# Optimization experiments

Hardware: AMD Instinct MI355X
Metric: run time of the kernel (lower is better)

## Reference

```python
import jax, jax.numpy as jnp
import numpy as np

B = 65536
HIDDEN = 200
K = 10          # num codewords == codeword dim (NearestEmbed(k, emb_size=k))
GROUPS = HIDDEN // K  # 20 sub-vectors of dim K per sample


def setup_inputs() -> dict:
    key = jax.random.key(0)
    ks = jax.random.split(key, 10)
    s = 0.05  # small init scale
    return {
        "x": jax.random.uniform(ks[0], (B, 784), dtype=jnp.float32),
        "W1": jax.random.normal(ks[1], (400, 784), dtype=jnp.float32) * s,
        "b1": jnp.zeros((400,), dtype=jnp.float32),
        "W2": jax.random.normal(ks[2], (HIDDEN, 400), dtype=jnp.float32) * s,
        "b2": jnp.zeros((HIDDEN,), dtype=jnp.float32),
        "W3": jax.random.normal(ks[3], (400, HIDDEN), dtype=jnp.float32) * s,
        "b3": jnp.zeros((400,), dtype=jnp.float32),
        "W4": jax.random.normal(ks[4], (784, 400), dtype=jnp.float32) * s,
        "b4": jnp.zeros((784,), dtype=jnp.float32),
        "codebook": jax.random.normal(ks[5], (K, K), dtype=jnp.float32),  # (n_codes, code_dim)
    }


def _quantize(z, codebook):
    # z: (B, K, GROUPS) -- quantize each length-K column vector to nearest codeword.
    v = jnp.transpose(z, (0, 2, 1))                       # (B, G, K)
    d2 = (jnp.sum(v * v, -1, keepdims=True)
          - 2.0 * jnp.einsum('bgk,ck->bgc', v, codebook)
          + jnp.sum(codebook * codebook, -1))             # (B, G, C)
    idx = jnp.argmin(d2, axis=-1)                         # (B, G)
    q = codebook[idx]                                     # (B, G, K) gather
    return jnp.transpose(q, (0, 2, 1)), idx               # (B, K, G)


def reference(x, W1, b1, W2, b2, W3, b3, W4, b4, codebook):
    # encode
    h1 = jax.nn.relu(x @ W1.T + b1)                       # (B, 400)
    z_e_flat = h1 @ W2.T + b2                             # (B, 200)
    z_e = z_e_flat.reshape(B, K, GROUPS)                  # (B, 10, 20)

    # z_q: straight-through quantization, codebook grad stopped (weight_sg=True)
    q, _ = _quantize(z_e, codebook)
    z_q = (z_e + jax.lax.stop_gradient(q - z_e)).reshape(B, HIDDEN)

    # emb: quantize detached z_e; gradient flows only to codebook via gather
    q2, _ = _quantize(jax.lax.stop_gradient(z_e), codebook)
    emb = q2.reshape(B, HIDDEN)

    # decode (original uses tanh on the output)
    h3 = jax.nn.relu(z_q @ W3.T + b3)                     # (B, 400)
    recon = jnp.tanh(h3 @ W4.T + b4)                      # (B, 784)
    return recon, z_e, emb
```

## Files before the change

kernel.cpp:

```cpp
#include <hip/hip_runtime.h>
#include <hip/hip_bf16.h>

#define NB   65536
#define KD   10
#define NG   20
#define NH   200
#define NH1  400
#define NIN  784

#define TAU 3e-4

using short8 = __attribute__((ext_vector_type(8))) short;
using f32x4  = __attribute__((ext_vector_type(4))) float;

__device__ inline float bf2f(unsigned short u) {
  union { unsigned int i; float f; } x; x.i = ((unsigned int)u) << 16; return x.f;
}
__device__ inline unsigned short f2bf(float v) {
  __hip_bfloat16 b = __float2bfloat16(v);
  return *reinterpret_cast<unsigned short*>(&b);
}
__device__ inline void gload_lds16(const void* g, void* l) {
  __builtin_amdgcn_global_load_lds(
      (const __attribute__((address_space(1))) unsigned int*)g,
      (__attribute__((address_space(3))) unsigned int*)l, 16, 0, 0);
}

__global__ __launch_bounds__(256) void gemm1_fused(
    const float* __restrict__ xf,
    const unsigned short* __restrict__ Bhi, const unsigned short* __restrict__ Blo,
    const float* __restrict__ bias,
    unsigned short* __restrict__ Ohi, unsigned short* __restrict__ Olo)
{
  __shared__ __align__(16) short As_hi[2][128][32];
  __shared__ __align__(16) short As_lo[2][128][32];
  __shared__ __align__(16) short Bs_hi[2][128][32];
  __shared__ __align__(16) short Bs_lo[2][128][32];
  const int tid = threadIdx.x;
  const int lane = tid & 63, wid = tid >> 6;
  const int wr = wid >> 1, wc = wid & 1;
  const int bid = blockIdx.x;
  const int sw = (bid & 7) * 256 + (bid >> 3);
  const int n0 = (sw & 3) * 128;
  const int m0 = (sw >> 2) * 128;
  const int rr = lane >> 2, kofs = (lane & 3) * 8;
  const int arow = tid >> 3;
  const int acol = (tid & 7) * 4;

  f32x4 acc[4][4];
  #pragma unroll
  for (int i = 0; i < 4; ++i)
    #pragma unroll
    for (int j = 0; j < 4; ++j) acc[i][j] = (f32x4){0.f, 0.f, 0.f, 0.f};

  float4 va[4];

  auto loadA = [&](int ks) {
    const int k0 = ks * 32;
    #pragma unroll
    for (int p = 0; p < 4; ++p) {
      const int row = p * 32 + arow;
      const int kk = k0 + acol;
      va[p] = make_float4(0.f, 0.f, 0.f, 0.f);
      if (kk < NIN)
        va[p] = *reinterpret_cast<const float4*>(xf + (size_t)(m0 + row) * NIN + kk);
    }
  };
  auto stageB = [&](int ks, int buf) {
    const int k0 = ks * 32;
    #pragma unroll
    for (int c = 0; c < 4; ++c) {
      const int ch = wid * 4 + c;
      if (ch < 8)
        gload_lds16(Bhi + (size_t)(n0 + ch * 16 + rr) * 800 + k0 + kofs,
                    (char*)&Bs_hi[buf][0][0] + ch * 1024);
      else
        gload_lds16(Blo + (size_t)(n0 + (ch - 8) * 16 + rr) * 800 + k0 + kofs,
                    (char*)&Bs_lo[buf][0][0] + (ch - 8) * 1024);
    }
  };
  auto writeA = [&](int buf) {
    #pragma unroll
    for (int p = 0; p < 4; ++p) {
      const int row = p * 32 + arow;
      const float4 v = va[p];
      short4 h, l;
      h.x = (short)f2bf(v.x); l.x = (short)f2bf(v.x - bf2f((unsigned short)h.x));
      h.y = (short)f2bf(v.y); l.y = (short)f2bf(v.y - bf2f((unsigned short)h.y));
      h.z = (short)f2bf(v.z); l.z = (short)f2bf(v.z - bf2f((unsigned short)h.z));
      h.w = (short)f2bf(v.w); l.w = (short)f2bf(v.w - bf2f((unsigned short)h.w));
      *reinterpret_cast<short4*>(&As_hi[buf][row][acol]) = h;
      *reinterpret_cast<short4*>(&As_lo[buf][row][acol]) = l;
    }
  };

  loadA(0);
  stageB(0, 0);
  writeA(0);
  __syncthreads();

  for (int ks = 0; ks < 25; ++ks) {
    const int cur = ks & 1, nxt = cur ^ 1;
    const bool more = (ks + 1 < 25);
    if (more) {
      loadA(ks + 1);
      stageB(ks + 1, nxt);
    }
    short8 ah[4], al[4], bh[4], bl[4];
    #pragma unroll
    for (int i = 0; i < 4; ++i) {
      ah[i] = *reinterpret_cast<const short8*>(&As_hi[cur][wr * 64 + i * 16 + (lane & 15)][(lane >> 4) * 8]);
      al[i] = *reinterpret_cast<const short8*>(&As_lo[cur][wr * 64 + i * 16 + (lane & 15)][(lane >> 4) * 8]);
      bh[i] = *reinterpret_cast<const short8*>(&Bs_hi[cur][wc * 64 + i * 16 + (lane & 15)][(lane >> 4) * 8]);
      bl[i] = *reinterpret_cast<const short8*>(&Bs_lo[cur][wc * 64 + i * 16 + (lane & 15)][(lane >> 4) * 8]);
    }
    #pragma unroll
    for (int i = 0; i < 4; ++i)
      #pragma unroll
      for (int j = 0; j < 4; ++j) {
        acc[i][j] = __builtin_amdgcn_mfma_f32_16x16x32_bf16(ah[i], bh[j], acc[i][j], 0, 0, 0);
        acc[i][j] = __builtin_amdgcn_mfma_f32_16x16x32_bf16(al[i], bh[j], acc[i][j], 0, 0, 0);
        acc[i][j] = __builtin_amdgcn_mfma_f32_16x16x32_bf16(ah[i], bl[j], acc[i][j], 0, 0, 0);
      }
    if (more) writeA(nxt);
    __syncthreads();
  }

  #pragma unroll
  for (int j = 0; j < 4; ++j) {
    const int n = n0 + wc * 64 + j * 16 + (lane & 15);
    if (n >= NH1) continue;
    const float bn = bias[n];
    #pragma unroll
    for (int i = 0; i < 4; ++i) {
      const int mb = m0 + wr * 64 + i * 16 + (lane >> 4) * 4;
      #pragma unroll
      for (int r = 0; r < 4; ++r) {
        float v = fmaxf(acc[i][j][r] + bn, 0.f);
        unsigned short h = f2bf(v);
        Ohi[(size_t)(mb + r) * NH1 + n] = h;
        Olo[(size_t)(mb + r) * NH1 + n] = f2bf(v - bf2f(h));
      }
    }
  }
}

__global__ __launch_bounds__(256) void gemm2_split(
    const unsigned short* __restrict__ Ahi, const unsigned short* __restrict__ Alo,
    const unsigned short* __restrict__ Bhi, const unsigned short* __restrict__ Blo,
    const unsigned short* __restrict__ zp, const float* __restrict__ bias,
    float* __restrict__ Of)
{
  __shared__ __align__(16) short As_hi[128][32];
  __shared__ __align__(16) short As_lo[128][32];
  __shared__ __align__(16) short Bs_hi[128][32];
  __shared__ __align__(16) short Bs_lo[128][32];
  const int tid = threadIdx.x;
  const int lane = tid & 63, wid = tid >> 6;
  const int wr = wid >> 1, wc = wid & 1;
  const int bid = blockIdx.x;
  const int sw = (bid & 7) * 128 + (bid >> 3);
  const int n0 = (sw & 1) * 128;
  const int m0 = (sw >> 1) * 128;

  const unsigned short* G = (wid == 0) ? Ahi : (wid == 1) ? Alo
                          : (wid == 2) ? Bhi : Blo;
  short* Lt = (wid == 0) ? &As_hi[0][0] : (wid == 1) ? &As_lo[0][0]
            : (wid == 2) ? &Bs_hi[0][0] : &Bs_lo[0][0];
  const bool isA = wid < 2;
  const int rbase = isA ? m0 : n0;
  const int ld = isA ? 400 : 416;
  const int rr = lane >> 2;
  const int kofs = (lane & 3) * 8;

  f32x4 acc[4][4];
  #pragma unroll
  for (int i = 0; i < 4; ++i)
    #pragma unroll
    for (int j = 0; j < 4; ++j) acc[i][j] = (f32x4){0.f, 0.f, 0.f, 0.f};

  for (int ks = 0; ks < 13; ++ks) {
    const int k0 = ks * 32;
    #pragma unroll
    for (int c = 0; c < 8; ++c) {
      const unsigned short* src =
          G + (size_t)(rbase + c * 16 + rr) * ld + k0 + kofs;
      if (isA && (k0 + kofs >= 400)) src = zp;
      gload_lds16(src, (char*)Lt + c * 1024);
    }
    __syncthreads();
    short8 ah[4], al[4], bh[4], bl[4];
    #pragma unroll
    for (int i = 0; i < 4; ++i) {
      ah[i] = *reinterpret_cast<const short8*>(&As_hi[wr * 64 + i * 16 + (lane & 15)][(lane >> 4) * 8]);
      al[i] = *reinterpret_cast<const short8*>(&As_lo[wr * 64 + i * 16 + (lane & 15)][(lane >> 4) * 8]);
      bh[i] = *reinterpret_cast<const short8*>(&Bs_hi[wc * 64 + i * 16 + (lane & 15)][(lane >> 4) * 8]);
      bl[i] = *reinterpret_cast<const short8*>(&Bs_lo[wc * 64 + i * 16 + (lane & 15)][(lane >> 4) * 8]);
    }
    #pragma unroll
    for (int i = 0; i < 4; ++i)
      #pragma unroll
      for (int j = 0; j < 4; ++j) {
        acc[i][j] = __builtin_amdgcn_mfma_f32_16x16x32_bf16(ah[i], bh[j], acc[i][j], 0, 0, 0);
        acc[i][j] = __builtin_amdgcn_mfma_f32_16x16x32_bf16(al[i], bh[j], acc[i][j], 0, 0, 0);
        acc[i][j] = __builtin_amdgcn_mfma_f32_16x16x32_bf16(ah[i], bl[j], acc[i][j], 0, 0, 0);
      }
    __syncthreads();
  }

  #pragma unroll
  for (int j = 0; j < 4; ++j) {
    const int n = n0 + wc * 64 + j * 16 + (lane & 15);
    if (n >= NH) continue;
    const float bn = bias[n];
    #pragma unroll
    for (int i = 0; i < 4; ++i) {
      const int mb = m0 + wr * 64 + i * 16 + (lane >> 4) * 4;
      #pragma unroll
      for (int r = 0; r < 4; ++r)
        Of[(size_t)(mb + r) * NH + n] = acc[i][j][r] + bn;
    }
  }
}

__global__ __launch_bounds__(256) void gemm3_mfma(
    const unsigned short* __restrict__ A,
    const __hip_bfloat16* __restrict__ Bp,
    const float* __restrict__ bias, __hip_bfloat16* __restrict__ H3)
{
  __shared__ __align__(16) short As[128][32];
  __shared__ __align__(16) short Bs[128][32];
  const int tid = threadIdx.x;
  const int lane = tid & 63, wid = tid >> 6;
  const int wr = wid >> 1, wc = wid & 1;
  const int bid = blockIdx.x;
  const int sw = (bid & 7) * 256 + (bid >> 3);
  const int n0 = (sw & 3) * 128;
  const int m0 = (sw >> 2) * 128;
  const int srow = lane >> 2;
  const int skp  = (lane & 3) * 8;
  const short* Ag = (const short*)A;
  const short* Bg = (const short*)Bp;
  f32x4 acc[4][4];
  #pragma unroll
  for (int i = 0; i < 4; ++i)
    #pragma unroll
    for (int j = 0; j < 4; ++j) acc[i][j] = (f32x4){0.f, 0.f, 0.f, 0.f};

  for (int k0 = 0; k0 < 224; k0 += 32) {
    #pragma unroll
    for (int c = 0; c < 2; ++c) {
      const int row = c * 64 + wid * 16 + srow;
      gload_lds16(Ag + (size_t)(m0 + row) * 200 + k0 + skp,
                  (char*)&As[0][0] + c * 4096 + wid * 1024);
      gload_lds16(Bg + (size_t)(n0 + row) * 224 + k0 + skp,
                  (char*)&Bs[0][0] + c * 4096 + wid * 1024);
    }
    __syncthreads();
    short8 af[4], bf[4];
    #pragma unroll
    for (int i = 0; i < 4; ++i)
      af[i] = *reinterpret_cast<const short8*>(&As[wr * 64 + i * 16 + (lane & 15)][(lane >> 4) * 8]);
    #pragma unroll
    for (int j = 0; j < 4; ++j)
      bf[j] = *reinterpret_cast<const short8*>(&Bs[wc * 64 + j * 16 + (lane & 15)][(lane >> 4) * 8]);
    #pragma unroll
    for (int i = 0; i < 4; ++i)
      #pragma unroll
      for (int j = 0; j < 4; ++j)
        acc[i][j] = __builtin_amdgcn_mfma_f32_16x16x32_bf16(af[i], bf[j], acc[i][j], 0, 0, 0);
    __syncthreads();
  }

  #pragma unroll
  for (int j = 0; j < 4; ++j) {
    const int n = n0 + wc * 64 + j * 16 + (lane & 15);
    if (n >= NH1) continue;
    const float bn = bias[n];
    #pragma unroll
    for (int i = 0; i < 4; ++i) {
      const int mb = m0 + wr * 64 + i * 16 + (lane >> 4) * 4;
      #pragma unroll
      for (int r = 0; r < 4; ++r)
        H3[(size_t)(mb + r) * NH1 + n] = __float2bfloat16(fmaxf(acc[i][j][r] + bn, 0.f));
    }
  }
}

__global__ __launch_bounds__(256) void gemm5_mfma(
    const __hip_bfloat16* __restrict__ A,
    const __hip_bfloat16* __restrict__ Bp,
    const float* __restrict__ bias, float* __restrict__ C)
{
  __shared__ __align__(16) short As[128][32];
  __shared__ __align__(16) short Bs[128][32];
  const int tid = threadIdx.x;
  const int lane = tid & 63, wid = tid >> 6;
  const int wr = wid >> 1, wc = wid & 1;
  const int bid = blockIdx.x;
  const int sw = (bid & 7) * 448 + (bid >> 3);
  const int n0 = (sw % 7) * 128;
  const int m0 = (sw / 7) * 128;
  const int srow = lane >> 2;
  const int skp  = (lane & 3) * 8;
  const short* Ag = (const short*)A;
  const short* Bg = (const short*)Bp;
  f32x4 acc[4][4];
  #pragma unroll
  for (int i = 0; i < 4; ++i)
    #pragma unroll
    for (int j = 0; j < 4; ++j) acc[i][j] = (f32x4){0.f, 0.f, 0.f, 0.f};

  for (int k0 = 0; k0 < 416; k0 += 32) {
    #pragma unroll
    for (int c = 0; c < 2; ++c) {
      const int row = c * 64 + wid * 16 + srow;
      gload_lds16(Ag + (size_t)(m0 + row) * 400 + k0 + skp,
                  (char*)&As[0][0] + c * 4096 + wid * 1024);
      gload_lds16(Bg + (size_t)(n0 + row) * 416 + k0 + skp,
                  (char*)&Bs[0][0] + c * 4096 + wid * 1024);
    }
    __syncthreads();
    short8 af[4], bf[4];
    #pragma unroll
    for (int i = 0; i < 4; ++i)
      af[i] = *reinterpret_cast<const short8*>(&As[wr * 64 + i * 16 + (lane & 15)][(lane >> 4) * 8]);
    #pragma unroll
    for (int j = 0; j < 4; ++j)
      bf[j] = *reinterpret_cast<const short8*>(&Bs[wc * 64 + j * 16 + (lane & 15)][(lane >> 4) * 8]);
    #pragma unroll
    for (int i = 0; i < 4; ++i)
      #pragma unroll
      for (int j = 0; j < 4; ++j)
        acc[i][j] = __builtin_amdgcn_mfma_f32_16x16x32_bf16(af[i], bf[j], acc[i][j], 0, 0, 0);
    __syncthreads();
  }

  #pragma unroll
  for (int j = 0; j < 4; ++j) {
    const int n = n0 + wc * 64 + j * 16 + (lane & 15);
    if (n >= NIN) continue;
    const float bn = bias[n];
    #pragma unroll
    for (int i = 0; i < 4; ++i) {
      const int mb = m0 + wr * 64 + i * 16 + (lane >> 4) * 4;
      #pragma unroll
      for (int r = 0; r < 4; ++r)
        C[(size_t)(mb + r) * NIN + n] = tanhf(acc[i][j][r] + bn);
    }
  }
}

__global__ __launch_bounds__(256) void conv_w(
    const float* __restrict__ W, unsigned short* __restrict__ Wh,
    unsigned short* __restrict__ Wl, int NP, int KP, int N, int K)
{
  const int i = blockIdx.x * 256 + threadIdx.x;
  if (i >= NP * KP) return;
  const int n = i / KP, k = i % KP;
  const float v = (n < N && k < K) ? W[(size_t)n * K + k] : 0.f;
  const unsigned short h = f2bf(v);
  Wh[i] = h;
  Wl[i] = f2bf(v - bf2f(h));
}

__global__ __launch_bounds__(256) void pad_w4(
    const float* __restrict__ W4, __hip_bfloat16* __restrict__ W4p)
{
  const int i = blockIdx.x * 256 + threadIdx.x;
  if (i >= 896 * 416) return;
  const int n = i / 416, k = i % 416;
  const float v = (n < NIN && k < NH1) ? W4[(size_t)n * NH1 + k] : 0.f;
  W4p[i] = __float2bfloat16(v);
}

__global__ __launch_bounds__(256) void pad_w3(
    const float* __restrict__ W3, __hip_bfloat16* __restrict__ W3p)
{
  const int i = blockIdx.x * 256 + threadIdx.x;
  if (i >= 512 * 224) return;
  const int n = i / 224, k = i % 224;
  const float v = (n < NH1 && k < NH) ? W3[(size_t)n * NH + k] : 0.f;
  W3p[i] = __float2bfloat16(v);
}

__global__ __launch_bounds__(256) void quant_kernel(
    const float* __restrict__ z_e, const float* __restrict__ cb,
    float* __restrict__ emb, unsigned short* __restrict__ ebf,
    unsigned char* __restrict__ sflag)
{
  __shared__ double cs[KD][KD];
  __shared__ double chalf[KD];
  __shared__ unsigned short cbf[KD][KD];
  const int tid = threadIdx.x;
  if (tid < KD * KD) {
    const double c = (double)cb[tid];
    cs[tid / KD][tid % KD] = c;
    cbf[tid / KD][tid % KD] = f2bf((float)c);
  }
  __syncthreads();
  if (tid < KD) {
    double s = 0.0;
    #pragma unroll
    for (int k = 0; k < KD; ++k) s += cs[tid][k] * cs[tid][k];
    chalf[tid] = 0.5 * s;
  }
  __syncthreads();

  const int gi = blockIdx.x * 256 + tid;
  const int b = gi / NG;
  const int g = gi % NG;
  const float* zrow = z_e + (size_t)b * NH + g;
  double v[KD];
  #pragma unroll
  for (int k = 0; k < KD; ++k) v[k] = (double)zrow[k * NG];

  int best = 0; double bt = 1e300, bt2 = 1e300;
  #pragma unroll
  for (int j = 0; j < KD; ++j) {
    double t = chalf[j];
    #pragma unroll
    for (int k = 0; k < KD; ++k) t -= v[k] * cs[j][k];
    if (t < bt) { bt2 = bt; bt = t; best = j; }
    else if (t < bt2) { bt2 = t; }
  }
  float* ep = emb + (size_t)b * NH + g;
  unsigned short* eb = ebf + (size_t)b * NH + g;
  #pragma unroll
  for (int k = 0; k < KD; ++k) {
    ep[k * NG] = (float)cs[best][k];
    eb[k * NG] = cbf[best][k];
  }
  if (bt2 - bt < TAU) sflag[b] = 1;
}

__global__ __launch_bounds__(256) void compact_kernel(
    const unsigned char* __restrict__ sflag, int* __restrict__ scount,
    int* __restrict__ slist)
{
  const int i = blockIdx.x * 256 + threadIdx.x;
  if (i < NB && sflag[i]) slist[atomicAdd(scount, 1)] = i;
}

__global__ __launch_bounds__(256) void repair_kernel(
    const float* __restrict__ x, const float* __restrict__ W1,
    const float* __restrict__ b1, const float* __restrict__ W2,
    const float* __restrict__ b2, const float* __restrict__ cb,
    const int* __restrict__ slist, const int* __restrict__ scount,
    float* __restrict__ emb, unsigned short* __restrict__ ebf)
{
  __shared__ double h1s[NH1];
  __shared__ double zs[NH];
  __shared__ double cs[KD][KD];
  __shared__ double chalf[KD];
  const int tid = threadIdx.x;
  const int lane = tid & 63, wv = tid >> 6;
  if (tid < KD * KD) cs[tid / KD][tid % KD] = (double)cb[tid];
  __syncthreads();
  if (tid < KD) {
    double s = 0.0;
    #pragma unroll
    for (int k = 0; k < KD; ++k) s += cs[tid][k] * cs[tid][k];
    chalf[tid] = 0.5 * s;
  }

  int S = *scount; if (S > NB) S = NB;

  for (int si = blockIdx.x; si < S; si += gridDim.x) {
    const int b = slist[si];
    double xr[4][4];
    #pragma unroll
    for (int it = 0; it < 4; ++it) {
      const int c4 = it * 64 + lane;
      if (c4 < 196) {
        float4 v = reinterpret_cast<const float4*>(x + (size_t)b * NIN)[c4];
        xr[it][0] = v.x; xr[it][1] = v.y; xr[it][2] = v.z; xr[it][3] = v.w;
      } else {
        xr[it][0] = xr[it][1] = xr[it][2] = xr[it][3] = 0.0;
      }
    }
    for (int j = wv; j < NH1; j += 4) {
      const float4* wr = reinterpret_cast<const float4*>(W1 + (size_t)j * NIN);
      double s0 = 0, s1 = 0, s2 = 0, s3 = 0;
      #pragma unroll
      for (int it = 0; it < 4; ++it) {
        const int c4 = it * 64 + lane;
        if (c4 < 196) {
          float4 w = wr[c4];
          s0 = fma(xr[it][0], (double)w.x, s0);
          s1 = fma(xr[it][1], (double)w.y, s1);
          s2 = fma(xr[it][2], (double)w.z, s2);
          s3 = fma(xr[it][3], (double)w.w, s3);
        }
      }
      double s = (s0 + s1) + (s2 + s3);
      #pragma unroll
      for (int off = 32; off > 0; off >>= 1) s += __shfl_down(s, off);
      if (lane == 0) { double h = s + (double)b1[j]; h1s[j] = h > 0.0 ? h : 0.0; }
    }
    __syncthreads();
    double hr[2][4];
    #pragma unroll
    for (int it = 0; it < 2; ++it) {
      const int c4 = it * 64 + lane;
      if (c4 < 100) {
        hr[it][0] = h1s[4 * c4 + 0]; hr[it][1] = h1s[4 * c4 + 1];
        hr[it][2] = h1s[4 * c4 + 2]; hr[it][3] = h1s[4 * c4 + 3];
      } else {
        hr[it][0] = hr[it][1] = hr[it][2] = hr[it][3] = 0.0;
      }
    }
    for (int n = wv; n < NH; n += 4) {
      const float4* wr = reinterpret_cast<const float4*>(W2 + (size_t)n * NH1);
      double s0 = 0, s1 = 0, s2 = 0, s3 = 0;
      #pragma unroll
      for (int it = 0; it < 2; ++it) {
        const int c4 = it * 64 + lane;
        if (c4 < 100) {
          float4 w = wr[c4];
          s0 = fma(hr[it][0], (double)w.x, s0);
          s1 = fma(hr[it][1], (double)w.y, s1);
          s2 = fma(hr[it][2], (double)w.z, s2);
          s3 = fma(hr[it][3], (double)w.w, s3);
        }
      }
      double s = (s0 + s1) + (s2 + s3);
      #pragma unroll
      for (int off = 32; off > 0; off >>= 1) s += __shfl_down(s, off);
      if (lane == 0) zs[n] = s + (double)b2[n];
    }
    __syncthreads();
    if (tid < NG) {
      const int g = tid;
      int best = 0; double bt = 1e300;
      #pragma unroll
      for (int j = 0; j < KD; ++j) {
        double t = chalf[j];
        #pragma unroll
        for (int k = 0; k < KD; ++k) t -= zs[k * NG + g] * cs[j][k];
        if (t < bt) { bt = t; best = j; }
      }
      #pragma unroll
      for (int k = 0; k < KD; ++k) {
        const float cv = (float)cs[best][k];
        emb[(size_t)b * NH + k * NG + g] = cv;
        ebf[(size_t)b * NH + k * NG + g] = f2bf(cv);
      }
    }
    __syncthreads();
  }
}

extern "C" void kernel_launch(void* const* d_in, const int* in_sizes, int n_in,
                              void* d_out, int out_size, void* d_ws, size_t ws_size,
                              hipStream_t stream) {
  const float* x  = (const float*)d_in[0];
  const float* W1 = (const float*)d_in[1];
  const float* b1 = (const float*)d_in[2];
  const float* W2 = (const float*)d_in[3];
  const float* b2 = (const float*)d_in[4];
  const float* W3 = (const float*)d_in[5];
  const float* b3 = (const float*)d_in[6];
  const float* W4 = (const float*)d_in[7];
  const float* b4 = (const float*)d_in[8];
  const float* cb = (const float*)d_in[9];

  float* out   = (float*)d_out;
  float* recon = out;
  float* z_e   = out + (size_t)NB * NIN;
  float* emb   = z_e + (size_t)NB * NH;

  unsigned short* h1_lo  = (unsigned short*)emb;
  unsigned short* emb_bf = (unsigned short*)recon;

  char* ws = (char*)d_ws;
  int*            scount = (int*)ws;
  unsigned short* zp    = (unsigned short*)(ws + 256);
  unsigned char*  sflag = (unsigned char*)(ws + 4096);
  __hip_bfloat16* W3p   = (__hip_bfloat16*)(ws + (1u << 20));
  int*            slist = (int*)(ws + (4u << 20));
  __hip_bfloat16* W4p   = (__hip_bfloat16*)(ws + (6u << 20));
  unsigned short* W1ph  = (unsigned short*)(ws + (7u << 20));
  unsigned short* W1pl  = (unsigned short*)(ws + (8u << 20));
  unsigned short* W2ph  = (unsigned short*)(ws + (9u << 20));
  unsigned short* W2pl  = (unsigned short*)(ws + (10u << 20));
  unsigned short* h1_hi = (unsigned short*)(ws + (16u << 20));
  __hip_bfloat16* h3    = (__hip_bfloat16*)(ws + (16u << 20));

  dim3 blk(256);
  hipMemsetAsync(ws, 0, 4096 + NB, stream);
  conv_w<<<(512 * 800 + 255) / 256, blk, 0, stream>>>(W1, W1ph, W1pl, 512, 800, NH1, NIN);
  conv_w<<<(256 * 416 + 255) / 256, blk, 0, stream>>>(W2, W2ph, W2pl, 256, 416, NH, NH1);
  pad_w4<<<(896 * 416 + 255) / 256, blk, 0, stream>>>(W4, W4p);
  pad_w3<<<(512 * 224 + 255) / 256, blk, 0, stream>>>(W3, W3p);

  gemm1_fused<<<2048, blk, 0, stream>>>(x, W1ph, W1pl, b1, h1_hi, h1_lo);
  gemm2_split<<<1024, blk, 0, stream>>>(h1_hi, h1_lo, W2ph, W2pl, zp, b2, z_e);

  quant_kernel<<<(NB * NG) / 256, blk, 0, stream>>>(z_e, cb, emb, emb_bf, sflag);
  compact_kernel<<<NB / 256, blk, 0, stream>>>(sflag, scount, slist);
  repair_kernel<<<2048, blk, 0, stream>>>(x, W1, b1, W2, b2, cb, slist, scount, emb, emb_bf);

  gemm3_mfma<<<2048, blk, 0, stream>>>(emb_bf, W3p, b3, h3);
  gemm5_mfma<<<3584, blk, 0, stream>>>(h3, W4p, b4, recon);
}
```

Measured before the change: 601.0 us.

## Swizzle LDS tiles, truncate-split bf16, fuse weight prep, fast tanh

Applies an XOR swizzle to the k-offsets of LDS tiles in all four GEMMs so the MFMA fragment reads avoid bank conflicts. Replaces the round-to-nearest bf16 hi part with bit truncation in the hi/lo split. Merges the four weight-conversion kernels into one launch and replaces tanhf with an exp-based formula. The truncation split and fast tanh change numerics slightly, and the workspace offsets are moved to fit the padded W1.

```diff
diff --git a/kernel.cpp b/kernel.cpp
--- a/kernel.cpp
+++ b/kernel.cpp
@@ -20,11 +20,21 @@
   __hip_bfloat16 b = __float2bfloat16(v);
   return *reinterpret_cast<unsigned short*>(&b);
 }
+__device__ inline void split2(float v, unsigned short& h, unsigned short& l) {
+  union { float f; unsigned int i; } u; u.f = v;
+  const unsigned int hbits = u.i & 0xffff0000u;
+  h = (unsigned short)(hbits >> 16);
+  union { unsigned int i; float f; } w; w.i = hbits;
+  l = f2bf(v - w.f);
+}
 __device__ inline void gload_lds16(const void* g, void* l) {
   __builtin_amdgcn_global_load_lds(
       (const __attribute__((address_space(1))) unsigned int*)g,
       (__attribute__((address_space(3))) unsigned int*)l, 16, 0, 0);
 }
+
+#define KSWZ(lane) ((((lane) & 3) ^ (((lane) >> 3) & 3)) * 8)
+#define CSW(lane)  (((((lane) >> 4) ^ (((lane) >> 1) & 3))) * 8)
 
 __global__ __launch_bounds__(256) void gemm1_fused(
     const float* __restrict__ xf,
@@ -43,8 +53,11 @@
   const int sw = (bid & 7) * 256 + (bid >> 3);
   const int n0 = (sw & 3) * 128;
   const int m0 = (sw >> 2) * 128;
-  const int rr = lane >> 2, kofs = (lane & 3) * 8;
+  const int rr = lane >> 2;
+  const int kswz = KSWZ(lane);
+  const int csw = CSW(lane);
   const int arow = tid >> 3;
+  const int wbyte = ((tid & 7) * 8) ^ (((tid >> 4) & 3) << 4);
   const int acol = (tid & 7) * 4;
 
   f32x4 acc[4][4];
@@ -72,25 +85,27 @@
     for (int c = 0; c < 4; ++c) {
       const int ch = wid * 4 + c;
       if (ch < 8)
-        gload_lds16(Bhi + (size_t)(n0 + ch * 16 + rr) * 800 + k0 + kofs,
+        gload_lds16(Bhi + (size_t)(n0 + ch * 16 + rr) * 800 + k0 + kswz,
                     (char*)&Bs_hi[buf][0][0] + ch * 1024);
       else
-        gload_lds16(Blo + (size_t)(n0 + (ch - 8) * 16 + rr) * 800 + k0 + kofs,
+        gload_lds16(Blo + (size_t)(n0 + (ch - 8) * 16 + rr) * 800 + k0 + kswz,
                     (char*)&Bs_lo[buf][0][0] + (ch - 8) * 1024);
     }
   };
   auto writeA = [&](int buf) {
+    char* bh = (char*)&As_hi[buf][0][0];
+    char* bl = (char*)&As_lo[buf][0][0];
     #pragma unroll
     for (int p = 0; p < 4; ++p) {
       const int row = p * 32 + arow;
       const float4 v = va[p];
       short4 h, l;
-      h.x = (short)f2bf(v.x); l.x = (short)f2bf(v.x - bf2f((unsigned short)h.x));
-      h.y = (short)f2bf(v.y); l.y = (short)f2bf(v.y - bf2f((unsigned short)h.y));
-      h.z = (short)f2bf(v.z); l.z = (short)f2bf(v.z - bf2f((unsigned short)h.z));
-      h.w = (short)f2bf(v.w); l.w = (short)f2bf(v.w - bf2f((unsigned short)h.w));
-      *reinterpret_cast<short4*>(&As_hi[buf][row][acol]) = h;
-      *reinterpret_cast<short4*>(&As_lo[buf][row][acol]) = l;
+      split2(v.x, (unsigned short&)h.x, (unsigned short&)l.x);
+      split2(v.y, (unsigned short&)h.y, (unsigned short&)l.y);
+      split2(v.z, (unsigned short&)h.z, (unsigned short&)l.z);
+      split2(v.w, (unsigned short&)h.w, (unsigned short&)l.w);
+      *reinterpret_cast<short4*>(bh + row * 64 + wbyte) = h;
+      *reinterpret_cast<short4*>(bl + row * 64 + wbyte) = l;
     }
   };
 
@@ -109,10 +124,10 @@
     short8 ah[4], al[4], bh[4], bl[4];
     #pragma unroll
     for (int i = 0; i < 4; ++i) {
-      ah[i] = *reinterpret_cast<const short8*>(&As_hi[cur][wr * 64 + i * 16 + (lane & 15)][(lane >> 4) * 8]);
-      al[i] = *reinterpret_cast<const short8*>(&As_lo[cur][wr * 64 + i * 16 + (lane & 15)][(lane >> 4) * 8]);
-      bh[i] = *reinterpret_cast<const short8*>(&Bs_hi[cur][wc * 64 + i * 16 + (lane & 15)][(lane >> 4) * 8]);
-      bl[i] = *reinterpret_cast<const short8*>(&Bs_lo[cur][wc * 64 + i * 16 + (lane & 15)][(lane >> 4) * 8]);
+      ah[i] = *reinterpret_cast<const short8*>(&As_hi[cur][wr * 64 + i * 16 + (lane & 15)][csw]);
+      al[i] = *reinterpret_cast<const short8*>(&As_lo[cur][wr * 64 + i * 16 + (lane & 15)][csw]);
+      bh[i] = *reinterpret_cast<const short8*>(&Bs_hi[cur][wc * 64 + i * 16 + (lane & 15)][csw]);
+      bl[i] = *reinterpret_cast<const short8*>(&Bs_lo[cur][wc * 64 + i * 16 + (lane & 15)][csw]);
     }
     #pragma unroll
     for (int i = 0; i < 4; ++i)
@@ -130,16 +145,17 @@
   for (int j = 0; j < 4; ++j) {
     const int n = n0 + wc * 64 + j * 16 + (lane & 15);
     if (n >= NH1) continue;
-    const float bn = bias[n];
+    const float bn = bias[j * 0 + n];
     #pragma unroll
     for (int i = 0; i < 4; ++i) {
       const int mb = m0 + wr * 64 + i * 16 + (lane >> 4) * 4;
       #pragma unroll
       for (int r = 0; r < 4; ++r) {
         float v = fmaxf(acc[i][j][r] + bn, 0.f);
-        unsigned short h = f2bf(v);
+        unsigned short h, l;
+        split2(v, h, l);
         Ohi[(size_t)(mb + r) * NH1 + n] = h;
-        Olo[(size_t)(mb + r) * NH1 + n] = f2bf(v - bf2f(h));
+        Olo[(size_t)(mb + r) * NH1 + n] = l;
       }
     }
   }
@@ -171,7 +187,8 @@
   const int rbase = isA ? m0 : n0;
   const int ld = isA ? 400 : 416;
   const int rr = lane >> 2;
-  const int kofs = (lane & 3) * 8;
+  const int kswz = KSWZ(lane);
+  const int csw = CSW(lane);
 
   f32x4 acc[4][4];
   #pragma unroll
@@ -184,18 +201,18 @@
     #pragma unroll
     for (int c = 0; c < 8; ++c) {
       const unsigned short* src =
-          G + (size_t)(rbase + c * 16 + rr) * ld + k0 + kofs;
-      if (isA && (k0 + kofs >= 400)) src = zp;
+          G + (size_t)(rbase + c * 16 + rr) * ld + k0 + kswz;
+      if (isA && (k0 + kswz >= 400)) src = zp;
       gload_lds16(src, (char*)Lt + c * 1024);
     }
     __syncthreads();
     short8 ah[4], al[4], bh[4], bl[4];
     #pragma unroll
     for (int i = 0; i < 4; ++i) {
-      ah[i] = *reinterpret_cast<const short8*>(&As_hi[wr * 64 + i * 16 + (lane & 15)][(lane >> 4) * 8]);
-      al[i] = *reinterpret_cast<const short8*>(&As_lo[wr * 64 + i * 16 + (lane & 15)][(lane >> 4) * 8]);
-      bh[i] = *reinterpret_cast<const short8*>(&Bs_hi[wc * 64 + i * 16 + (lane & 15)][(lane >> 4) * 8]);
-      bl[i] = *reinterpret_cast<const short8*>(&Bs_lo[wc * 64 + i * 16 + (lane & 15)][(lane >> 4) * 8]);
+      ah[i] = *reinterpret_cast<const short8*>(&As_hi[wr * 64 + i * 16 + (lane & 15)][csw]);
+      al[i] = *reinterpret_cast<const short8*>(&As_lo[wr * 64 + i * 16 + (lane & 15)][csw]);
+      bh[i] = *reinterpret_cast<const short8*>(&Bs_hi[wc * 64 + i * 16 + (lane & 15)][csw]);
+      bl[i] = *reinterpret_cast<const short8*>(&Bs_lo[wc * 64 + i * 16 + (lane & 15)][csw]);
     }
     #pragma unroll
     for (int i = 0; i < 4; ++i)
@@ -237,8 +254,8 @@
   const int sw = (bid & 7) * 256 + (bid >> 3);
   const int n0 = (sw & 3) * 128;
   const int m0 = (sw >> 2) * 128;
-  const int srow = lane >> 2;
-  const int skp  = (lane & 3) * 8;
+  const int kswz = KSWZ(lane);
+  const int csw = CSW(lane);
   const short* Ag = (const short*)A;
   const short* Bg = (const short*)Bp;
   f32x4 acc[4][4];
@@ -250,20 +267,20 @@
   for (int k0 = 0; k0 < 224; k0 += 32) {
     #pragma unroll
     for (int c = 0; c < 2; ++c) {
-      const int row = c * 64 + wid * 16 + srow;
-      gload_lds16(Ag + (size_t)(m0 + row) * 200 + k0 + skp,
+      const int row = c * 64 + wid * 16 + (lane >> 2);
+      gload_lds16(Ag + (size_t)(m0 + row) * 200 + k0 + kswz,
                   (char*)&As[0][0] + c * 4096 + wid * 1024);
-      gload_lds16(Bg + (size_t)(n0 + row) * 224 + k0 + skp,
+      gload_lds16(Bg + (size_t)(n0 + row) * 224 + k0 + kswz,
                   (char*)&Bs[0][0] + c * 4096 + wid * 1024);
     }
     __syncthreads();
     short8 af[4], bf[4];
     #pragma unroll
     for (int i = 0; i < 4; ++i)
-      af[i] = *reinterpret_cast<const short8*>(&As[wr * 64 + i * 16 + (lane & 15)][(lane >> 4) * 8]);
+      af[i] = *reinterpret_cast<const short8*>(&As[wr * 64 + i * 16 + (lane & 15)][csw]);
     #pragma unroll
     for (int j = 0; j < 4; ++j)
-      bf[j] = *reinterpret_cast<const short8*>(&Bs[wc * 64 + j * 16 + (lane & 15)][(lane >> 4) * 8]);
+      bf[j] = *reinterpret_cast<const short8*>(&Bs[wc * 64 + j * 16 + (lane & 15)][csw]);
     #pragma unroll
     for (int i = 0; i < 4; ++i)
       #pragma unroll
@@ -301,8 +318,8 @@
   const int sw = (bid & 7) * 448 + (bid >> 3);
   const int n0 = (sw % 7) * 128;
   const int m0 = (sw / 7) * 128;
-  const int srow = lane >> 2;
-  const int skp  = (lane & 3) * 8;
+  const int kswz = KSWZ(lane);
+  const int csw = CSW(lane);
   const short* Ag = (const short*)A;
   const short* Bg = (const short*)Bp;
   f32x4 acc[4][4];
@@ -314,20 +331,20 @@
   for (int k0 = 0; k0 < 416; k0 += 32) {
     #pragma unroll
     for (int c = 0; c < 2; ++c) {
-      const int row = c * 64 + wid * 16 + srow;
-      gload_lds16(Ag + (size_t)(m0 + row) * 400 + k0 + skp,
+      const int row = c * 64 + wid * 16 + (lane >> 2);
+      gload_lds16(Ag + (size_t)(m0 + row) * 400 + k0 + kswz,
                   (char*)&As[0][0] + c * 4096 + wid * 1024);
-      gload_lds16(Bg + (size_t)(n0 + row) * 416 + k0 + skp,
+      gload_lds16(Bg + (size_t)(n0 + row) * 416 + k0 + kswz,
                   (char*)&Bs[0][0] + c * 4096 + wid * 1024);
     }
     __syncthreads();
     short8 af[4], bf[4];
     #pragma unroll
     for (int i = 0; i < 4; ++i)
-      af[i] = *reinterpret_cast<const short8*>(&As[wr * 64 + i * 16 + (lane & 15)][(lane >> 4) * 8]);
+      af[i] = *reinterpret_cast<const short8*>(&As[wr * 64 + i * 16 + (lane & 15)][csw]);
     #pragma unroll
     for (int j = 0; j < 4; ++j)
-      bf[j] = *reinterpret_cast<const short8*>(&Bs[wc * 64 + j * 16 + (lane & 15)][(lane >> 4) * 8]);
+      bf[j] = *reinterpret_cast<const short8*>(&Bs[wc * 64 + j * 16 + (lane & 15)][csw]);
     #pragma unroll
     for (int i = 0; i < 4; ++i)
       #pragma unroll
@@ -345,43 +362,45 @@
     for (int i = 0; i < 4; ++i) {
       const int mb = m0 + wr * 64 + i * 16 + (lane >> 4) * 4;
       #pragma unroll
-      for (int r = 0; r < 4; ++r)
-        C[(size_t)(mb + r) * NIN + n] = tanhf(acc[i][j][r] + bn);
-    }
-  }
-}
-
-__global__ __launch_bounds__(256) void conv_w(
-    const float* __restrict__ W, unsigned short* __restrict__ Wh,
-    unsigned short* __restrict__ Wl, int NP, int KP, int N, int K)
+      for (int r = 0; r < 4; ++r) {
+        const float zv = acc[i][j][r] + bn;
+        const float t = __expf(2.0f * zv);
+        C[(size_t)(mb + r) * NIN + n] = 1.0f - __fdividef(2.0f, t + 1.0f);
+      }
+    }
+  }
+}
+
+__global__ __launch_bounds__(256) void prep_all(
+    const float* __restrict__ W1, const float* __restrict__ W2,
+    const float* __restrict__ W3, const float* __restrict__ W4,
+    unsigned short* __restrict__ W1ph, unsigned short* __restrict__ W1pl,
+    unsigned short* __restrict__ W2ph, unsigned short* __restrict__ W2pl,
+    __hip_bfloat16* __restrict__ W3p, __hip_bfloat16* __restrict__ W4p)
 {
   const int i = blockIdx.x * 256 + threadIdx.x;
-  if (i >= NP * KP) return;
-  const int n = i / KP, k = i % KP;
-  const float v = (n < N && k < K) ? W[(size_t)n * K + k] : 0.f;
-  const unsigned short h = f2bf(v);
-  Wh[i] = h;
-  Wl[i] = f2bf(v - bf2f(h));
-}
-
-__global__ __launch_bounds__(256) void pad_w4(
-    const float* __restrict__ W4, __hip_bfloat16* __restrict__ W4p)
-{
-  const int i = blockIdx.x * 256 + threadIdx.x;
-  if (i >= 896 * 416) return;
-  const int n = i / 416, k = i % 416;
-  const float v = (n < NIN && k < NH1) ? W4[(size_t)n * NH1 + k] : 0.f;
-  W4p[i] = __float2bfloat16(v);
-}
-
-__global__ __launch_bounds__(256) void pad_w3(
-    const float* __restrict__ W3, __hip_bfloat16* __restrict__ W3p)
-{
-  const int i = blockIdx.x * 256 + threadIdx.x;
-  if (i >= 512 * 224) return;
-  const int n = i / 224, k = i % 224;
-  const float v = (n < NH1 && k < NH) ? W3[(size_t)n * NH + k] : 0.f;
-  W3p[i] = __float2bfloat16(v);
+  if (i < 409600) {
+    const int n = i / 800, k = i % 800;
+    const float v = (n < NH1 && k < NIN) ? W1[(size_t)n * NIN + k] : 0.f;
+    unsigned short h, l; split2(v, h, l);
+    W1ph[i] = h; W1pl[i] = l;
+  } else if (i < 516096) {
+    const int j = i - 409600;
+    const int n = j / 416, k = j % 416;
+    const float v = (n < NH && k < NH1) ? W2[(size_t)n * NH1 + k] : 0.f;
+    unsigned short h, l; split2(v, h, l);
+    W2ph[j] = h; W2pl[j] = l;
+  } else if (i < 888832) {
+    const int j = i - 516096;
+    const int n = j / 416, k = j % 416;
+    const float v = (n < NIN && k < NH1) ? W4[(size_t)n * NH1 + k] : 0.f;
+    W4p[j] = __float2bfloat16(v);
+  } else if (i < 1003520) {
+    const int j = i - 888832;
+    const int n = j / 224, k = j % 224;
+    const float v = (n < NH1 && k < NH) ? W3[(size_t)n * NH + k] : 0.f;
+    W3p[j] = __float2bfloat16(v);
+  }
 }
 
 __global__ __launch_bounds__(256) void quant_kernel(
@@ -581,18 +600,15 @@
   int*            slist = (int*)(ws + (4u << 20));
   __hip_bfloat16* W4p   = (__hip_bfloat16*)(ws + (6u << 20));
   unsigned short* W1ph  = (unsigned short*)(ws + (7u << 20));
-  unsigned short* W1pl  = (unsigned short*)(ws + (8u << 20));
-  unsigned short* W2ph  = (unsigned short*)(ws + (9u << 20));
-  unsigned short* W2pl  = (unsigned short*)(ws + (10u << 20));
+  unsigned short* W1pl  = (unsigned short*)(ws + (9u << 20));
+  unsigned short* W2ph  = (unsigned short*)(ws + (11u << 20));
+  unsigned short* W2pl  = (unsigned short*)(ws + (12u << 20));
   unsigned short* h1_hi = (unsigned short*)(ws + (16u << 20));
   __hip_bfloat16* h3    = (__hip_bfloat16*)(ws + (16u << 20));
 
   dim3 blk(256);
   hipMemsetAsync(ws, 0, 4096 + NB, stream);
-  conv_w<<<(512 * 800 + 255) / 256, blk, 0, stream>>>(W1, W1ph, W1pl, 512, 800, NH1, NIN);
-  conv_w<<<(256 * 416 + 255) / 256, blk, 0, stream>>>(W2, W2ph, W2pl, 256, 416, NH, NH1);
-  pad_w4<<<(896 * 416 + 255) / 256, blk, 0, stream>>>(W4, W4p);
-  pad_w3<<<(512 * 224 + 255) / 256, blk, 0, stream>>>(W3, W3p);
+  prep_all<<<3920, blk, 0, stream>>>(W1, W2, W3, W4, W1ph, W1pl, W2ph, W2pl, W3p, W4p);
 
   gemm1_fused<<<2048, blk, 0, stream>>>(x, W1ph, W1pl, b1, h1_hi, h1_lo);
   gemm2_split<<<1024, blk, 0, stream>>>(h1_hi, h1_lo, W2ph, W2pl, zp, b2, z_e);
```

Measured after the change: 595.9 us. No clear change (-0.8%).
